# Performance work log

Measured on AMD Instinct MI355X. Metric: run time of the kernel, lower is better.

The kernel has to match this reference:

```python
import jax, jax.numpy as jnp
import numpy as np

EPS = 1e-5
MAX_NORM = 1.0 - 1e-4

def _artanh(x):
    x = jnp.clip(x, -1.0 + 1e-5, 1.0 - 1e-5)
    return 0.5 * (jnp.log1p(x) - jnp.log1p(-x))

def _norm(x):
    return jnp.sqrt(jnp.maximum(jnp.sum(x * x, axis=-1, keepdims=True), EPS * EPS))

def _project(x):
    # clip points into the Poincare ball (c=1)
    n = _norm(x)
    return x * jnp.minimum(1.0, MAX_NORM / n)

def _logmap0(x):
    n = _norm(x)
    return _artanh(n) * x / n

def _expmap0(v):
    n = _norm(v)
    return jnp.tanh(n) * v / n

def _mobius_add(x, y):
    x2 = jnp.sum(x * x, -1, keepdims=True)
    y2 = jnp.sum(y * y, -1, keepdims=True)
    xy = jnp.sum(x * y, -1, keepdims=True)
    num = (1.0 + 2.0 * xy + y2) * x + (1.0 - x2) * y
    den = 1.0 + 2.0 * xy + x2 * y2
    return num / jnp.maximum(den, EPS)

def _mobius_matvec_all(W, x):
    # x: [B,T,D] on ball, W: [K,D,D] -> [B,T,K,D] (mx = x @ W[k].T for each expert k)
    mx = jnp.einsum('btd,ked->btke', x, W)
    xn = _norm(x)[:, :, None, :]            # [B,T,1,1]
    mn = _norm(mx)                          # [B,T,K,1]
    return jnp.tanh(mn / xn * _artanh(xn)) * mx / mn

def _depthwise_conv1d(x, w, b):
    # x: [B,T,C], w: [C,1,3] depthwise, padding=1
    y = jax.lax.conv_general_dilated(
        jnp.transpose(x, (0, 2, 1)), w, (1,), 'SAME',
        feature_group_count=x.shape[-1],
        dimension_numbers=('NCW', 'OIW', 'NCW'))
    return jnp.transpose(y, (0, 2, 1)) + b

def setup_inputs() -> dict:
    key = jax.random.key(0)
    ks = jax.random.split(key, 10)
    B, T, V, D, K, E, R = 8, 512, 50257, 64, 17, 32, 40
    return {
        'tokens': jax.random.randint(ks[0], (B, T), 0, V),
        'token_embed': 0.02 * jax.random.normal(ks[1], (V, D), jnp.float32),
        'conv_w': 0.3 * jax.random.normal(ks[2], (D, 1, 3), jnp.float32),
        'conv_b': jnp.zeros((D,), jnp.float32),
        'lin_w': 0.1 * jax.random.normal(ks[3], (D, K), jnp.float32),
        'lin_b': jnp.zeros((K,), jnp.float32),
        'exp_W': (1.0 / 8.0) * jax.random.normal(ks[4], (K, D, D), jnp.float32),
        'exp_bias': 0.01 * jax.random.normal(ks[5], (K, D), jnp.float32),
        'ln_gamma': jnp.ones((K, E), jnp.float32),
        'ln_beta': jnp.zeros((K, E), jnp.float32),
        'rel_T': jax.random.normal(ks[6], (R, E, E), jnp.float32),
        'rel_S': jax.random.normal(ks[7], (R, E, E), jnp.float32),
    }

def reference(tokens, token_embed, conv_w, conv_b, lin_w, lin_b,
              exp_W, exp_bias, ln_gamma, ln_beta, rel_T, rel_S):
    B, T = tokens.shape
    h0 = token_embed[tokens]                                  # [B,T,64]
    # TinyPosRouter: depthwise conv -> linear -> log_softmax
    hc = _depthwise_conv1d(h0, conv_w, conv_b)
    logp = jax.nn.log_softmax(hc @ lin_w + lin_b, axis=-1)    # [B,T,17]
    p = jnp.exp(logp)
    # round-trip through tangent space (as in source)
    x = _expmap0(_logmap0(_project(h0)))                      # [B,T,64]
    # all 17 hyperbolic experts, batched
    mv = _mobius_matvec_all(exp_W, x)                         # [B,T,17,64]
    y = _project(_mobius_add(mv, _project(exp_bias)))         # mobius bias add
    yt = _logmap0(y)                                          # tangent [B,T,17,64]
    a, g = jnp.split(yt, 2, axis=-1)
    y_glu = a * jax.nn.sigmoid(g)                             # [B,T,17,32]
    mu = jnp.mean(y_glu, -1, keepdims=True)
    var = jnp.var(y_glu, -1, keepdims=True)
    y_ln = (y_glu - mu) / jnp.sqrt(var + 1e-5) * ln_gamma + ln_beta
    y_out = _expmap0(y_ln)                                    # [B,T,17,32]
    y_avg = jnp.einsum('btke,btk->bte', y_out, p)             # soft routing
    # per-relation biaffine scores
    Th = jnp.einsum('btd,rde->brte', y_avg, rel_T)            # [B,40,T,32]
    Sd = jnp.einsum('btd,rde->brte', y_avg, rel_S)
    scores = jnp.einsum('brid,brjd->brij', Th, Sd) / Th.shape[-1]  # [B,40,T,T]
    score_rel = jnp.max(scores, axis=1)                       # [B,T,T]
    score_rel = jnp.where(jnp.eye(T, dtype=bool)[None], -1e9, score_rel)
    # greedy arborescence approximation: each dependent picks max-scoring head
    tree = jnp.argmax(score_rel, axis=1)                      # [B,T]
    return tree, score_rel, logp
```

## Files before the change

kernel.cpp:

```cpp
#include <hip/hip_runtime.h>
#include <hip/hip_bf16.h>
#include <math.h>

#define EPS   1e-5f
#define EPS2  (1e-5f * 1e-5f)
#define MAXN  (1.0f - 1e-4f)

typedef __attribute__((ext_vector_type(8))) short bf16x8;
typedef __attribute__((ext_vector_type(4))) float f32x4;

__device__ __forceinline__ float artanh_(float x) {
    x = fminf(fmaxf(x, -1.0f + 1e-5f), 1.0f - 1e-5f);
    return 0.5f * (log1pf(x) - log1pf(-x));
}
__device__ __forceinline__ float redw(float v) {
    #pragma unroll
    for (int m = 32; m >= 1; m >>= 1) v += __shfl_xor(v, m);
    return v;
}
__device__ __forceinline__ float red16(float v) {
    v += __shfl_xor(v, 1); v += __shfl_xor(v, 2);
    v += __shfl_xor(v, 4); v += __shfl_xor(v, 8);
    return v;
}
__device__ __forceinline__ float red8(float v) {
    v += __shfl_xor(v, 1); v += __shfl_xor(v, 2); v += __shfl_xor(v, 4);
    return v;
}
__device__ __forceinline__ float sigmoid_(float z) { return 1.0f / (1.0f + expf(-z)); }
__device__ __forceinline__ ushort f2bf(float f) {
    union { __hip_bfloat16 b; ushort u; } cv;
    cv.b = __float2bfloat16(f);
    return cv.u;
}
__device__ __forceinline__ bf16x8 pack8(float4 lo, float4 hi) {
    bf16x8 r;
    r[0] = (short)f2bf(lo.x); r[1] = (short)f2bf(lo.y);
    r[2] = (short)f2bf(lo.z); r[3] = (short)f2bf(lo.w);
    r[4] = (short)f2bf(hi.x); r[5] = (short)f2bf(hi.y);
    r[6] = (short)f2bf(hi.z); r[7] = (short)f2bf(hi.w);
    return r;
}

__global__ __launch_bounds__(256) void k1_token(
    const int* __restrict__ tokens, const float* __restrict__ emb,
    const float* __restrict__ conv_w, const float* __restrict__ conv_b,
    const float* __restrict__ lin_w, const float* __restrict__ lin_b,
    float* __restrict__ x_out, float* __restrict__ xn_out,
    float* __restrict__ p_out, float* __restrict__ logp_out)
{
    const int tok = blockIdx.x * 4 + (threadIdx.x >> 6);
    const int t   = tok & 511;
    const int c   = threadIdx.x & 63;

    const int id0 = tokens[tok];
    float h0 = emb[id0 * 64 + c];
    float hm = 0.0f, hp = 0.0f;
    if (t > 0)   hm = emb[tokens[tok - 1] * 64 + c];
    if (t < 511) hp = emb[tokens[tok + 1] * 64 + c];

    float hc = conv_w[c * 3 + 0] * hm + conv_w[c * 3 + 1] * h0 +
               conv_w[c * 3 + 2] * hp + conv_b[c];

    float myLg = 0.0f;
    #pragma unroll
    for (int j = 0; j < 17; ++j) {
        float v = redw(hc * lin_w[c * 17 + j]);
        if (c == j) myLg = v + lin_b[j];
    }
    float mx = (c < 17) ? myLg : -1e30f;
    #pragma unroll
    for (int m = 32; m >= 1; m >>= 1) mx = fmaxf(mx, __shfl_xor(mx, m));
    float ev = (c < 17) ? expf(myLg - mx) : 0.0f;
    float se = redw(ev);
    float lse = logf(se);
    if (c < 17) {
        float lp = myLg - mx - lse;
        logp_out[tok * 17 + c] = lp;
        p_out[tok * 17 + c]    = expf(lp);
    }

    float n0 = sqrtf(fmaxf(redw(h0 * h0), EPS2));
    float xp = h0 * fminf(1.0f, MAXN / n0);
    float n1 = sqrtf(fmaxf(redw(xp * xp), EPS2));
    float v1 = artanh_(n1) / n1 * xp;
    float n2 = sqrtf(fmaxf(redw(v1 * v1), EPS2));
    float xv = tanhf(n2) / n2 * v1;

    x_out[tok * 64 + c] = xv;
    float n3 = sqrtf(fmaxf(redw(xv * xv), EPS2));
    if (c == 0) xn_out[tok] = n3;
}

__global__ __launch_bounds__(256) void k2_expert(
    const float* __restrict__ x_in, const float* __restrict__ xn_in,
    const float* __restrict__ p_in, const float* __restrict__ expW,
    const float* __restrict__ expB, const float* __restrict__ g_in,
    const float* __restrict__ b_in, __hip_bfloat16* __restrict__ yk_out)
{
    __shared__ float mv_s[16][65];
    __shared__ float pb[64];
    __shared__ float gsk[32], bsk[32];
    __shared__ float p_sk[16];
    __shared__ float xn_s[16], axn_s[16];
    __shared__ float y2s_s;

    const int tid = threadIdx.x;
    const int l = tid & 63, w = tid >> 6;
    const int tg = tid >> 4, eg = tid & 15;
    const int k = blockIdx.x >> 8;
    const int chunk = blockIdx.x & 255;
    const int tok0 = chunk * 16;

    {
        const int d0 = (l >> 4) * 8;
        const float* ap = x_in + (tok0 + (l & 15)) * 64 + d0;
        const float* bp = expW + k * 4096 + (16 * w + (l & 15)) * 64 + d0;
        bf16x8 a0 = pack8(*reinterpret_cast<const float4*>(ap),
                          *reinterpret_cast<const float4*>(ap + 4));
        bf16x8 a1 = pack8(*reinterpret_cast<const float4*>(ap + 32),
                          *reinterpret_cast<const float4*>(ap + 36));
        bf16x8 b0 = pack8(*reinterpret_cast<const float4*>(bp),
                          *reinterpret_cast<const float4*>(bp + 4));
        bf16x8 b1 = pack8(*reinterpret_cast<const float4*>(bp + 32),
                          *reinterpret_cast<const float4*>(bp + 36));
        f32x4 acc = {0.f, 0.f, 0.f, 0.f};
        acc = __builtin_amdgcn_mfma_f32_16x16x32_bf16(a0, b0, acc, 0, 0, 0);
        acc = __builtin_amdgcn_mfma_f32_16x16x32_bf16(a1, b1, acc, 0, 0, 0);
        #pragma unroll
        for (int q = 0; q < 4; ++q)
            mv_s[(l >> 4) * 4 + q][16 * w + (l & 15)] = acc[q];
    }

    if (tid < 64) {
        float wv = expB[k * 64 + tid];
        float s = redw(wv * wv);
        float n = sqrtf(fmaxf(s, EPS2));
        float sc = fminf(1.0f, MAXN / n);
        pb[tid] = wv * sc;
        if (tid == 0) y2s_s = s * sc * sc;
    }
    if (tid >= 64 && tid < 96)  gsk[tid - 64] = g_in[k * 32 + (tid - 64)];
    if (tid >= 96 && tid < 128) bsk[tid - 96] = b_in[k * 32 + (tid - 96)];
    if (tid >= 128 && tid < 144) p_sk[tid - 128] = p_in[(tok0 + tid - 128) * 17 + k];
    if (tid >= 144 && tid < 160) {
        float xn = xn_in[tok0 + tid - 144];
        xn_s[tid - 144] = xn;
        axn_s[tid - 144] = artanh_(xn);
    }
    __syncthreads();

    const float xnv = xn_s[tg], axnv = axn_s[tg];
    float4 mvq = *reinterpret_cast<const float4*>(&mv_s[tg][eg * 4]);
    float mv0 = mvq.x, mv1 = mvq.y, mv2 = mvq.z, mv3 = mvq.w;

    float mn = sqrtf(fmaxf(red16(mv0*mv0 + mv1*mv1 + mv2*mv2 + mv3*mv3), EPS2));
    float tv = tanhf(mn / xnv * axnv);
    float cf = tv / mn;
    float xa0 = cf * mv0, xa1 = cf * mv1, xa2 = cf * mv2, xa3 = cf * mv3;
    float x2 = tv * tv;

    float4 pbv = *reinterpret_cast<const float4*>(&pb[eg * 4]);
    float xy = red16(xa0*pbv.x + xa1*pbv.y + xa2*pbv.z + xa3*pbv.w);
    float y2 = y2s_s;
    float ca = 1.0f + 2.0f * xy + y2;
    float cb = 1.0f - x2;
    float den = fmaxf(1.0f + 2.0f * xy + x2 * y2, EPS);
    float rden = 1.0f / den;
    float y0 = (ca * xa0 + cb * pbv.x) * rden;
    float y1 = (ca * xa1 + cb * pbv.y) * rden;
    float y2c = (ca * xa2 + cb * pbv.z) * rden;
    float y3 = (ca * xa3 + cb * pbv.w) * rden;

    float s2 = red16(y0*y0 + y1*y1 + y2c*y2c + y3*y3);
    float nP = sqrtf(fmaxf(s2, EPS2));
    float scP = fminf(1.0f, MAXN / nP);
    y0 *= scP; y1 *= scP; y2c *= scP; y3 *= scP;

    float n2 = sqrtf(fmaxf(s2 * scP * scP, EPS2));
    float lc = artanh_(n2) / n2;
    float yt0 = lc * y0, yt1 = lc * y1, yt2 = lc * y2c, yt3 = lc * y3;

    float pr0 = __shfl_xor(yt0, 8), pr1 = __shfl_xor(yt1, 8);
    float pr2 = __shfl_xor(yt2, 8), pr3 = __shfl_xor(yt3, 8);
    float gl0, gl1, gl2, gl3;
    if (eg < 8) {
        gl0 = yt0 * sigmoid_(pr0); gl1 = yt1 * sigmoid_(pr1);
        gl2 = yt2 * sigmoid_(pr2); gl3 = yt3 * sigmoid_(pr3);
    } else {
        gl0 = pr0 * sigmoid_(yt0); gl1 = pr1 * sigmoid_(yt1);
        gl2 = pr2 * sigmoid_(yt2); gl3 = pr3 * sigmoid_(yt3);
    }

    float mu = red8(gl0 + gl1 + gl2 + gl3) * (1.0f / 32.0f);
    float sq = red8(gl0*gl0 + gl1*gl1 + gl2*gl2 + gl3*gl3) * (1.0f / 32.0f);
    float rstd = rsqrtf(fmaxf(sq - mu * mu, 0.0f) + 1e-5f);
    int c0 = 4 * (eg & 7);
    float ln0 = (gl0 - mu) * rstd * gsk[c0 + 0] + bsk[c0 + 0];
    float ln1 = (gl1 - mu) * rstd * gsk[c0 + 1] + bsk[c0 + 1];
    float ln2 = (gl2 - mu) * rstd * gsk[c0 + 2] + bsk[c0 + 2];
    float ln3 = (gl3 - mu) * rstd * gsk[c0 + 3] + bsk[c0 + 3];

    float n3 = sqrtf(fmaxf(red8(ln0*ln0 + ln1*ln1 + ln2*ln2 + ln3*ln3), EPS2));
    float tc = tanhf(n3) / n3;

    float pk = p_sk[tg];
    float wq = pk * tc;

    if (eg < 8) {
        int tok = tok0 + tg;
        ushort4 o;
        o.x = f2bf(wq * ln0);
        o.y = f2bf(wq * ln1);
        o.z = f2bf(wq * ln2);
        o.w = f2bf(wq * ln3);
        *reinterpret_cast<ushort4*>(
            reinterpret_cast<ushort*>(yk_out) + ((size_t)tok * 17 + k) * 32 + c0) = o;
    }
}

__global__ __launch_bounds__(256) void k3_reduce(
    const __hip_bfloat16* __restrict__ yk, ushort* __restrict__ yab)
{
    int idx = blockIdx.x * 256 + threadIdx.x;
    int tok = idx >> 5, e = idx & 31;
    const __hip_bfloat16* p = yk + (size_t)tok * 17 * 32 + e;
    float s = 0.0f;
    #pragma unroll
    for (int k = 0; k < 17; ++k) s += __bfloat162float(p[k * 32]);
    yab[idx] = f2bf(s);
}

__global__ __launch_bounds__(256) void k4_rel(
    const ushort* __restrict__ yab, const float* __restrict__ relT,
    const float* __restrict__ relS, ushort* __restrict__ Z,
    unsigned long long* __restrict__ pmax)
{
    const int blk = blockIdx.x;
    const int b = blk / 160;
    const int rem = blk % 160;
    const int r = rem >> 2, tq = rem & 3;
    __shared__ float Ts[32][33], Ss[32][33], Mm[32][33];
    __shared__ float Zb[128][33];
    const int tid = threadIdx.x;
    const int l = tid & 63, w = tid >> 6;

    if (r == 0 && tid < 128)
        pmax[(size_t)b * 512 + tq * 128 + tid] = 0ull;

    {
        int d = tid >> 3, e0 = (tid & 7) * 4;
        float4 wT = *reinterpret_cast<const float4*>(&relT[r * 1024 + tid * 4]);
        float4 wS = *reinterpret_cast<const float4*>(&relS[r * 1024 + tid * 4]);
        Ts[d][e0 + 0] = wT.x; Ts[d][e0 + 1] = wT.y;
        Ts[d][e0 + 2] = wT.z; Ts[d][e0 + 3] = wT.w;
        Ss[d][e0 + 0] = wS.x; Ss[d][e0 + 1] = wS.y;
        Ss[d][e0 + 2] = wS.z; Ss[d][e0 + 3] = wS.w;
    }
    __syncthreads();

    {
        int d = tid >> 3, dp0 = (tid & 7) * 4;
        float m0 = 0.f, m1 = 0.f, m2 = 0.f, m3 = 0.f;
        #pragma unroll
        for (int e = 0; e < 32; ++e) {
            float tvv = Ts[d][e];
            m0 = fmaf(tvv, Ss[dp0 + 0][e], m0);
            m1 = fmaf(tvv, Ss[dp0 + 1][e], m1);
            m2 = fmaf(tvv, Ss[dp0 + 2][e], m2);
            m3 = fmaf(tvv, Ss[dp0 + 3][e], m3);
        }
        Mm[d][dp0 + 0] = m0; Mm[d][dp0 + 1] = m1;
        Mm[d][dp0 + 2] = m2; Mm[d][dp0 + 3] = m3;
    }
    __syncthreads();

    bf16x8 bm0, bm1;
    #pragma unroll
    for (int i = 0; i < 8; ++i) {
        int d = (l >> 4) * 8 + i;
        bm0[i] = (short)f2bf(Mm[d][(l & 15)]);
        bm1[i] = (short)f2bf(Mm[d][16 + (l & 15)]);
    }

    #pragma unroll
    for (int s = 0; s < 2; ++s) {
        int trow = tq * 128 + (w * 2 + s) * 16 + (l & 15);
        bf16x8 a = *reinterpret_cast<const bf16x8*>(
            yab + ((size_t)(b * 512) + trow) * 32 + (l >> 4) * 8);
        f32x4 acc0 = {0.f, 0.f, 0.f, 0.f}, acc1 = {0.f, 0.f, 0.f, 0.f};
        acc0 = __builtin_amdgcn_mfma_f32_16x16x32_bf16(a, bm0, acc0, 0, 0, 0);
        acc1 = __builtin_amdgcn_mfma_f32_16x16x32_bf16(a, bm1, acc1, 0, 0, 0);
        #pragma unroll
        for (int q = 0; q < 4; ++q) {
            int lr = (w * 2 + s) * 16 + (l >> 4) * 4 + q;
            Zb[lr][(l & 15)]      = acc0[q];
            Zb[lr][16 + (l & 15)] = acc1[q];
        }
    }
    __syncthreads();

    {
        int t2 = tid >> 1, half = tid & 1;
        union { ushort u[16]; uint4 q[2]; } pk;
        #pragma unroll
        for (int j = 0; j < 16; ++j) pk.u[j] = f2bf(Zb[t2][half * 16 + j]);
        size_t off = ((size_t)(b * 40 + r) * 512 + tq * 128 + t2) * 32 + half * 16;
        *reinterpret_cast<uint4*>(Z + off)     = pk.q[0];
        *reinterpret_cast<uint4*>(Z + off + 8) = pk.q[1];
    }
}

__global__ __launch_bounds__(1024) void k5_scores(
    const ushort* __restrict__ Z, const ushort* __restrict__ yab,
    float* __restrict__ score_out, unsigned long long* __restrict__ pmax)
{
    __shared__ float L[4][64][64];
    __shared__ unsigned long long pk_s[16][64];

    const int blk = blockIdx.x;
    const int b = blk >> 6, tile = blk & 63;
    const int it = (tile >> 3) * 64, jt = (tile & 7) * 64;
    const int w = threadIdx.x >> 6, lane = threadIdx.x & 63;
    const int q = w >> 2, s = w & 3;
    const int i0 = it + s * 16;
    const int arow = i0 + (lane & 15);
    const int koff = (lane >> 4) * 8;

    bf16x8 bb[4];
    #pragma unroll
    for (int c = 0; c < 4; ++c) {
        int jrow = jt + c * 16 + (lane & 15);
        bb[c] = *reinterpret_cast<const bf16x8*>(
            yab + ((size_t)(b * 512) + jrow) * 32 + koff);
    }

    f32x4 runmax[4];
    #pragma unroll
    for (int c = 0; c < 4; ++c)
        #pragma unroll
        for (int qq = 0; qq < 4; ++qq) runmax[c][qq] = -3.0e38f;

    const int r0 = q * 10;
    #pragma unroll 2
    for (int r = r0; r < r0 + 10; ++r) {
        bf16x8 a = *reinterpret_cast<const bf16x8*>(
            Z + ((size_t)(b * 40 + r) * 512 + arow) * 32 + koff);
        #pragma unroll
        for (int c = 0; c < 4; ++c) {
            f32x4 acc = {0.f, 0.f, 0.f, 0.f};
            acc = __builtin_amdgcn_mfma_f32_16x16x32_bf16(a, bb[c], acc, 0, 0, 0);
            #pragma unroll
            for (int qq = 0; qq < 4; ++qq) runmax[c][qq] = fmaxf(runmax[c][qq], acc[qq]);
        }
    }

    #pragma unroll
    for (int c = 0; c < 4; ++c) {
        #pragma unroll
        for (int qq = 0; qq < 4; ++qq) {
            int li = s * 16 + (lane >> 4) * 4 + qq;
            int lj = c * 16 + (lane & 15);
            L[q][li][lj] = runmax[c][qq];
        }
    }
    __syncthreads();

    {
        const int jl = threadIdx.x & 63, ig = threadIdx.x >> 6;
        const int gj = jt + jl;
        float bestv = -3.0e38f; int besti = it;
        #pragma unroll
        for (int p = 0; p < 4; ++p) {
            int i = ig + p * 16;
            float v = fmaxf(fmaxf(L[0][i][jl], L[1][i][jl]),
                            fmaxf(L[2][i][jl], L[3][i][jl])) * (1.0f / 32.0f);
            int gi = it + i;
            if (gi == gj) v = -1e9f;
            score_out[((size_t)b * 512 + gi) * 512 + gj] = v;
            if (v > bestv) { bestv = v; besti = gi; }
        }
        unsigned int ub = __float_as_uint(bestv);
        unsigned int ok = (ub >> 31) ? ~ub : (ub | 0x80000000u);
        pk_s[ig][jl] = ((unsigned long long)ok << 32) | (unsigned int)(511 - besti);
    }
    __syncthreads();
    if (threadIdx.x < 64) {
        unsigned long long best = pk_s[0][threadIdx.x];
        #pragma unroll
        for (int g = 1; g < 16; ++g) {
            unsigned long long v = pk_s[g][threadIdx.x];
            if (v > best) best = v;
        }
        atomicMax(&pmax[(size_t)b * 512 + jt + threadIdx.x], best);
    }
}

__global__ __launch_bounds__(256) void k6_tree(
    const unsigned long long* __restrict__ pmax, float* __restrict__ tree)
{
    int idx = blockIdx.x * 256 + threadIdx.x;
    tree[idx] = (float)(511 - (int)(pmax[idx] & 0x1ffull));
}

extern "C" void kernel_launch(void* const* d_in, const int* in_sizes, int n_in,
                              void* d_out, int out_size, void* d_ws, size_t ws_size,
                              hipStream_t stream)
{
    const int*   tokens  = (const int*)  d_in[0];
    const float* emb     = (const float*)d_in[1];
    const float* conv_w  = (const float*)d_in[2];
    const float* conv_b  = (const float*)d_in[3];
    const float* lin_w   = (const float*)d_in[4];
    const float* lin_b   = (const float*)d_in[5];
    const float* expW    = (const float*)d_in[6];
    const float* expB    = (const float*)d_in[7];
    const float* ln_g    = (const float*)d_in[8];
    const float* ln_b    = (const float*)d_in[9];
    const float* relT    = (const float*)d_in[10];
    const float* relS    = (const float*)d_in[11];

    float* out = (float*)d_out;
    float* tree_out  = out;
    float* score_out = out + 4096;
    float* logp_out  = out + 4096 + 2097152;

    float* ws = (float*)d_ws;
    float* x_ws  = ws;
    float* xn_ws = ws + 262144;
    float* p_ws  = ws + 266240;
    ushort* yab_ws = (ushort*)(ws + 335872);
    __hip_bfloat16* yk_ws = (__hip_bfloat16*)(ws + 401408);
    ushort* Z_ws = (ushort*)(ws + 1515520);
    unsigned long long* pmax_ws =
        (unsigned long long*)(ws + 4136960);

    k1_token<<<1024, 256, 0, stream>>>(tokens, emb, conv_w, conv_b, lin_w, lin_b,
                                       x_ws, xn_ws, p_ws, logp_out);
    k2_expert<<<4352, 256, 0, stream>>>(x_ws, xn_ws, p_ws, expW, expB, ln_g, ln_b, yk_ws);
    k3_reduce<<<512, 256, 0, stream>>>(yk_ws, yab_ws);
    k4_rel<<<1280, 256, 0, stream>>>(yab_ws, relT, relS, Z_ws, pmax_ws);
    k5_scores<<<512, 1024, 0, stream>>>(Z_ws, yab_ws, score_out, pmax_ws);
    k6_tree<<<16, 256, 0, stream>>>(pmax_ws, tree_out);
}
```

Before: 72.40 us.

## Use fast exp/log intrinsics and fold tree kernel into scores via last-block counter

Replaces log1pf/tanhf/expf/logf with __expf/__logf-based formulations in the token and expert kernels to cut transcendental instruction cost. Separately removes the k6_tree launch by having the last k5 block per batch, detected with an atomic counter reset in k4, read the packed argmax and write the tree output. This saves one kernel launch but adds a threadfence and atomic per block, and the fast intrinsics reduce accuracy slightly.

```diff
diff --git a/kernel.cpp b/kernel.cpp
--- a/kernel.cpp
+++ b/kernel.cpp
@@ -11,7 +11,11 @@
 
 __device__ __forceinline__ float artanh_(float x) {
     x = fminf(fmaxf(x, -1.0f + 1e-5f), 1.0f - 1e-5f);
-    return 0.5f * (log1pf(x) - log1pf(-x));
+    return 0.5f * __logf((1.0f + x) / (1.0f - x));
+}
+__device__ __forceinline__ float tanh_pos(float x) {
+    float t = __expf(-2.0f * x);
+    return (1.0f - t) / (1.0f + t);
 }
 __device__ __forceinline__ float redw(float v) {
     #pragma unroll
@@ -27,7 +31,7 @@
     v += __shfl_xor(v, 1); v += __shfl_xor(v, 2); v += __shfl_xor(v, 4);
     return v;
 }
-__device__ __forceinline__ float sigmoid_(float z) { return 1.0f / (1.0f + expf(-z)); }
+__device__ __forceinline__ float sigmoid_(float z) { return 1.0f / (1.0f + __expf(-z)); }
 __device__ __forceinline__ ushort f2bf(float f) {
     union { __hip_bfloat16 b; ushort u; } cv;
     cv.b = __float2bfloat16(f);
@@ -71,13 +75,13 @@
     float mx = (c < 17) ? myLg : -1e30f;
     #pragma unroll
     for (int m = 32; m >= 1; m >>= 1) mx = fmaxf(mx, __shfl_xor(mx, m));
-    float ev = (c < 17) ? expf(myLg - mx) : 0.0f;
+    float ev = (c < 17) ? __expf(myLg - mx) : 0.0f;
     float se = redw(ev);
-    float lse = logf(se);
+    float lse = __logf(se);
     if (c < 17) {
         float lp = myLg - mx - lse;
         logp_out[tok * 17 + c] = lp;
-        p_out[tok * 17 + c]    = expf(lp);
+        p_out[tok * 17 + c]    = __expf(lp);
     }
 
     float n0 = sqrtf(fmaxf(redw(h0 * h0), EPS2));
@@ -85,7 +89,7 @@
     float n1 = sqrtf(fmaxf(redw(xp * xp), EPS2));
     float v1 = artanh_(n1) / n1 * xp;
     float n2 = sqrtf(fmaxf(redw(v1 * v1), EPS2));
-    float xv = tanhf(n2) / n2 * v1;
+    float xv = tanh_pos(n2) / n2 * v1;
 
     x_out[tok * 64 + c] = xv;
     float n3 = sqrtf(fmaxf(redw(xv * xv), EPS2));
@@ -155,7 +159,7 @@
     float mv0 = mvq.x, mv1 = mvq.y, mv2 = mvq.z, mv3 = mvq.w;
 
     float mn = sqrtf(fmaxf(red16(mv0*mv0 + mv1*mv1 + mv2*mv2 + mv3*mv3), EPS2));
-    float tv = tanhf(mn / xnv * axnv);
+    float tv = tanh_pos(mn / xnv * axnv);
     float cf = tv / mn;
     float xa0 = cf * mv0, xa1 = cf * mv1, xa2 = cf * mv2, xa3 = cf * mv3;
     float x2 = tv * tv;
@@ -202,7 +206,7 @@
     float ln3 = (gl3 - mu) * rstd * gsk[c0 + 3] + bsk[c0 + 3];
 
     float n3 = sqrtf(fmaxf(red8(ln0*ln0 + ln1*ln1 + ln2*ln2 + ln3*ln3), EPS2));
-    float tc = tanhf(n3) / n3;
+    float tc = tanh_pos(n3) / n3;
 
     float pk = p_sk[tg];
     float wq = pk * tc;
@@ -234,7 +238,7 @@
 __global__ __launch_bounds__(256) void k4_rel(
     const ushort* __restrict__ yab, const float* __restrict__ relT,
     const float* __restrict__ relS, ushort* __restrict__ Z,
-    unsigned long long* __restrict__ pmax)
+    unsigned long long* __restrict__ pmax, unsigned int* __restrict__ cnt)
 {
     const int blk = blockIdx.x;
     const int b = blk / 160;
@@ -247,6 +251,8 @@
 
     if (r == 0 && tid < 128)
         pmax[(size_t)b * 512 + tq * 128 + tid] = 0ull;
+    if (rem == 0 && tid == 128)
+        cnt[b] = 0u;
 
     {
         int d = tid >> 3, e0 = (tid & 7) * 4;
@@ -313,10 +319,12 @@
 
 __global__ __launch_bounds__(1024) void k5_scores(
     const ushort* __restrict__ Z, const ushort* __restrict__ yab,
-    float* __restrict__ score_out, unsigned long long* __restrict__ pmax)
+    float* __restrict__ score_out, unsigned long long* __restrict__ pmax,
+    unsigned int* __restrict__ cnt, float* __restrict__ tree)
 {
     __shared__ float L[4][64][64];
     __shared__ unsigned long long pk_s[16][64];
+    __shared__ unsigned int last_s;
 
     const int blk = blockIdx.x;
     const int b = blk >> 6, tile = blk & 63;
@@ -394,13 +402,14 @@
         }
         atomicMax(&pmax[(size_t)b * 512 + jt + threadIdx.x], best);
     }
-}
-
-__global__ __launch_bounds__(256) void k6_tree(
-    const unsigned long long* __restrict__ pmax, float* __restrict__ tree)
-{
-    int idx = blockIdx.x * 256 + threadIdx.x;
-    tree[idx] = (float)(511 - (int)(pmax[idx] & 0x1ffull));
+
+    __syncthreads();
+    if (threadIdx.x == 0) { __threadfence(); last_s = atomicAdd(&cnt[b], 1u); }
+    __syncthreads();
+    if (last_s == 63u && threadIdx.x < 512) {
+        unsigned long long key = atomicMax(&pmax[(size_t)b * 512 + threadIdx.x], 0ull);
+        tree[b * 512 + threadIdx.x] = (float)(511 - (int)(key & 0x1ffull));
+    }
 }
 
 extern "C" void kernel_launch(void* const* d_in, const int* in_sizes, int n_in,
@@ -434,12 +443,12 @@
     ushort* Z_ws = (ushort*)(ws + 1515520);
     unsigned long long* pmax_ws =
         (unsigned long long*)(ws + 4136960);
+    unsigned int* cnt_ws = (unsigned int*)(ws + 4145152);
 
     k1_token<<<1024, 256, 0, stream>>>(tokens, emb, conv_w, conv_b, lin_w, lin_b,
                                        x_ws, xn_ws, p_ws, logp_out);
     k2_expert<<<4352, 256, 0, stream>>>(x_ws, xn_ws, p_ws, expW, expB, ln_g, ln_b, yk_ws);
     k3_reduce<<<512, 256, 0, stream>>>(yk_ws, yab_ws);
-    k4_rel<<<1280, 256, 0, stream>>>(yab_ws, relT, relS, Z_ws, pmax_ws);
-    k5_scores<<<512, 1024, 0, stream>>>(Z_ws, yab_ws, score_out, pmax_ws);
-    k6_tree<<<16, 256, 0, stream>>>(pmax_ws, tree_out);
-}
+    k4_rel<<<1280, 256, 0, stream>>>(yab_ws, relT, relS, Z_ws, pmax_ws, cnt_ws);
+    k5_scores<<<512, 1024, 0, stream>>>(Z_ws, yab_ws, score_out, pmax_ws, cnt_ws, tree_out);
+}
```

Result: slower. 81.24 us (+12.2%).
